# Kernel optimization log

Hardware: AMD Instinct MI355X
Metric: run time of the kernel (lower is better)

Reference implementation:

```python
import math
import jax, jax.numpy as jnp
import numpy as np

D_MODEL = 1024
D_FF = 4096
NUM_EXPERTS = 8
CAPACITY_FACTOR = 1.0
ALPHA = 0.01
Z_LOSS_COEF = 0.001


def setup_inputs() -> dict:
    key = jax.random.key(0)
    kx, kr, k1, k2, kb1, kb2 = jax.random.split(key, 6)
    init_scale = 0.1
    x = jax.random.normal(kx, (8, 2048, D_MODEL), dtype=jnp.float32)
    # torch Linear weight [out,in] with truncated-normal std=init_scale*sqrt(1/fan_in);
    # stored here in math layout: y = x @ W
    w_router = jax.random.normal(kr, (D_MODEL, NUM_EXPERTS), jnp.float32) * (init_scale * math.sqrt(1.0 / D_MODEL))
    w1 = jax.random.normal(k1, (NUM_EXPERTS, D_MODEL, D_FF), jnp.float32) * (init_scale * math.sqrt(1.0 / D_MODEL))
    w2 = jax.random.normal(k2, (NUM_EXPERTS, D_FF, D_MODEL), jnp.float32) * (init_scale * math.sqrt(1.0 / D_FF))
    b1 = jnp.zeros((NUM_EXPERTS, D_FF), jnp.float32)
    b2 = jnp.zeros((NUM_EXPERTS, D_MODEL), jnp.float32)
    return {"x": x, "w_router": w_router, "w1": w1, "b1": b1, "w2": w2, "b2": b2}


def reference(x, w_router, w1, b1, w2, b2):
    # Eval-mode forward (no router noise, no dropout), as in is_training=False.
    d = x.shape[-1]
    E = w1.shape[0]
    tokens = x.reshape(-1, d)                       # [T, d]
    T = tokens.shape[0]

    router_logits = tokens @ w_router               # [T, E]
    router_probs = jax.nn.softmax(router_logits.astype(jnp.float32), axis=-1)
    top1_prob = jnp.max(router_probs, axis=-1)      # [T]
    top1_idx = jnp.argmax(router_probs, axis=-1)    # [T]

    # load-balancing aux loss
    counts = jnp.zeros((E,), jnp.float32).at[top1_idx].add(1.0)
    fi = jax.lax.stop_gradient(counts / T)
    Pi = router_probs.mean(axis=0)
    aux_loss = ALPHA * E * jnp.dot(fi, Pi)
    z_loss = jnp.mean(jnp.square(jax.scipy.special.logsumexp(router_logits, axis=-1)))
    aux_loss = aux_loss + Z_LOSS_COEF * z_loss

    # capacity-limited first-come-first-serve positions per expert
    C = max(int(math.ceil(T / float(E) * CAPACITY_FACTOR)), 1)
    onehot = (top1_idx[:, None] == jnp.arange(E)[None, :]).astype(jnp.int32)  # [T, E]
    cum = jnp.cumsum(onehot, axis=0)
    pos = jnp.take_along_axis(cum, top1_idx[:, None], axis=1)[:, 0] - 1       # [T]
    fits = pos < C                                                            # [T]
    pos_c = jnp.clip(pos, 0, C - 1)

    # dispatch: dropped tokens contribute zeros (collision-safe add)
    contrib = tokens * fits[:, None].astype(tokens.dtype)
    expert_inputs = jnp.zeros((E, C, d), tokens.dtype).at[top1_idx, pos_c].add(contrib)

    # per-expert FFN as batched GEMMs
    h = jax.nn.relu(jnp.einsum('ecd,edf->ecf', expert_inputs, w1) + b1[:, None, :])
    expert_outputs = jnp.einsum('ecf,efd->ecd', h, w2) + b2[:, None, :]       # [E, C, d]

    # combine: fitted tokens get prob-weighted expert output, dropped tokens pass through
    gathered = expert_outputs[top1_idx, pos_c]                                # [T, d]
    scaled = gathered * top1_prob[:, None].astype(gathered.dtype)
    outputs_tokens = jnp.where(fits[:, None], scaled, tokens)
    return outputs_tokens.reshape(x.shape), aux_loss
```

## Files before the change

### kernel.cpp

```cpp
#include <hip/hip_runtime.h>
#include <stdint.h>
#include <stddef.h>

typedef __attribute__((ext_vector_type(4))) float floatx4;
typedef __attribute__((ext_vector_type(8))) int intx8;

#define T_TOK 16384
#define DM 1024
#define DF 4096
#define NE 8
#define CAP 2048

#define SCALE_ONE 127
#define SCALE_W   121

static __device__ __forceinline__ int pk4(float a, float b, float c, float d) {
  int v = __builtin_amdgcn_cvt_pk_fp8_f32(a, b, 0, false);
  v = __builtin_amdgcn_cvt_pk_fp8_f32(c, d, v, true);
  return v;
}

static __device__ __forceinline__ void async_cp16(const void* g, void* l) {
  typedef const unsigned int __attribute__((address_space(1)))* gp_t;
  typedef unsigned int __attribute__((address_space(3)))* lp_t;
  __builtin_amdgcn_global_load_lds((gp_t)g, (lp_t)l, 16, 0, 0);
}

__global__ void init_kernel(int* __restrict__ src_token) {
  int i = blockIdx.x * 256 + threadIdx.x;
  if (i < NE * CAP) src_token[i] = -1;
}

__global__ void __launch_bounds__(256, 4) router_kernel(
    const float* __restrict__ x, const float* __restrict__ wr,
    int* __restrict__ top_idx, float* __restrict__ top_prob,
    float* __restrict__ part) {
  __shared__ float wl[8][1024];
  __shared__ float bstat[4][12];
  int tid = threadIdx.x;
  int lane = tid & 63, w = tid >> 6;

#pragma unroll
  for (int r = 0; r < 8; r++) {
    int j = tid + 256 * r;
    float4 v = ((const float4*)wr)[j];
    int f = j >> 1;
    int e0 = (j & 1) * 4;
    wl[e0 + 0][f] = v.x;
    wl[e0 + 1][f] = v.y;
    wl[e0 + 2][f] = v.z;
    wl[e0 + 3][f] = v.w;
  }
  __syncthreads();

  int t0 = blockIdx.x * 8 + w * 2;

  float4 xa[2][4];
#pragma unroll
  for (int tok = 0; tok < 2; tok++)
#pragma unroll
    for (int i = 0; i < 4; i++)
      xa[tok][i] = *(const float4*)&x[(size_t)(t0 + tok) * DM + i * 256 + lane * 4];

  float acc[2][8];
#pragma unroll
  for (int tok = 0; tok < 2; tok++)
#pragma unroll
    for (int e = 0; e < 8; e++) acc[tok][e] = 0.f;

#pragma unroll
  for (int i = 0; i < 4; i++) {
    float4 wv[8];
#pragma unroll
    for (int e = 0; e < 8; e++)
      wv[e] = *(const float4*)&wl[e][i * 256 + lane * 4];
#pragma unroll
    for (int tok = 0; tok < 2; tok++) {
      float4 xv = xa[tok][i];
#pragma unroll
      for (int e = 0; e < 8; e++)
        acc[tok][e] = fmaf(xv.x, wv[e].x,
                      fmaf(xv.y, wv[e].y,
                      fmaf(xv.z, wv[e].z,
                      fmaf(xv.w, wv[e].w, acc[tok][e]))));
    }
  }

  float pi_acc[8] = {0, 0, 0, 0, 0, 0, 0, 0};
  float z_acc = 0.f;
#pragma unroll
  for (int tok = 0; tok < 2; tok++) {
    float a[8];
#pragma unroll
    for (int e = 0; e < 8; e++) a[e] = acc[tok][e];
#pragma unroll
    for (int off = 32; off > 0; off >>= 1)
#pragma unroll
      for (int e = 0; e < 8; e++) a[e] += __shfl_xor(a[e], off, 64);
    float mx = a[0]; int mi = 0;
#pragma unroll
    for (int e = 1; e < 8; e++) { if (a[e] > mx) { mx = a[e]; mi = e; } }
    float s = 0.f, pr[8];
#pragma unroll
    for (int e = 0; e < 8; e++) { pr[e] = __expf(a[e] - mx); s += pr[e]; }
    float inv = 1.f / s;
#pragma unroll
    for (int e = 0; e < 8; e++) pi_acc[e] += pr[e] * inv;
    float lse = mx + __logf(s);
    z_acc += lse * lse;
    if (lane == 0) { top_idx[t0 + tok] = mi; top_prob[t0 + tok] = pr[mi] * inv; }
  }

  if (lane == 0) {
#pragma unroll
    for (int e = 0; e < 8; e++) bstat[w][e] = pi_acc[e];
    bstat[w][8] = z_acc;
  }
  __syncthreads();
  if (tid < 9) {
    float s = bstat[0][tid] + bstat[1][tid] + bstat[2][tid] + bstat[3][tid];
    part[(size_t)blockIdx.x * 16 + tid] = s;
  }
}

__global__ void __launch_bounds__(1024) scan_kernel(
    const int* __restrict__ top_idx, const float* __restrict__ part,
    int* __restrict__ dest_slot, int* __restrict__ src_token,
    float* __restrict__ aux_out) {
  __shared__ int cnt[1024 * 9];
  __shared__ float sstat[16][12];
  int tid = threadIdx.x;

  float ps[9];
#pragma unroll
  for (int e = 0; e < 9; e++) ps[e] = 0.f;
#pragma unroll
  for (int rr = 0; rr < 2; rr++) {
    const float* pp = &part[(size_t)(tid + rr * 1024) * 16];
#pragma unroll
    for (int e = 0; e < 9; e++) ps[e] += pp[e];
  }
#pragma unroll
  for (int off = 32; off > 0; off >>= 1)
#pragma unroll
    for (int e = 0; e < 9; e++) ps[e] += __shfl_xor(ps[e], off, 64);
  if ((tid & 63) == 0) {
#pragma unroll
    for (int e = 0; e < 9; e++) sstat[tid >> 6][e] = ps[e];
  }

  int eloc[16];
  int c[8] = {0, 0, 0, 0, 0, 0, 0, 0};
#pragma unroll
  for (int i = 0; i < 16; i++) {
    int e = top_idx[tid * 16 + i];
    eloc[i] = e;
    c[e]++;
  }
#pragma unroll
  for (int e = 0; e < 8; e++) cnt[tid * 9 + e] = c[e];
  __syncthreads();
  for (int s = 1; s < 1024; s <<= 1) {
    int v[8];
    if (tid >= s) {
#pragma unroll
      for (int e = 0; e < 8; e++) v[e] = cnt[(tid - s) * 9 + e];
    }
    __syncthreads();
    if (tid >= s) {
#pragma unroll
      for (int e = 0; e < 8; e++) cnt[tid * 9 + e] += v[e];
    }
    __syncthreads();
  }
  int run[8];
#pragma unroll
  for (int e = 0; e < 8; e++) run[e] = cnt[tid * 9 + e] - c[e];
#pragma unroll
  for (int i = 0; i < 16; i++) {
    int t = tid * 16 + i;
    int e = eloc[i];
    int pos = run[e]++;
    int d = (pos < CAP) ? (e * CAP + pos) : -1;
    dest_slot[t] = d;
    if (d >= 0) src_token[d] = t;
  }
  if (tid == 1023) {
    float st[9];
#pragma unroll
    for (int e = 0; e < 9; e++) {
      float s = 0.f;
      for (int ww = 0; ww < 16; ww++) s += sstat[ww][e];
      st[e] = s;
    }
    float aux = 0.f;
    for (int e = 0; e < 8; e++)
      aux += ((float)cnt[1023 * 9 + e] / (float)T_TOK) * (st[e] / (float)T_TOK);
    aux = 0.01f * 8.f * aux + 0.001f * (st[8] / (float)T_TOK);
    *aux_out = aux;
  }
}

__global__ void __launch_bounds__(256) dispatch_kernel(
    const float* __restrict__ x, const int* __restrict__ src_token,
    unsigned char* __restrict__ A) {
  int slot = blockIdx.x;
  int tid = threadIdx.x;
  int src = src_token[slot];
  int v = 0;
  if (src >= 0) {
    float4 xv = *(const float4*)&x[(size_t)src * DM + tid * 4];
    v = pk4(xv.x, xv.y, xv.z, xv.w);
  }
  *(int*)&A[(size_t)slot * DM + tid * 4] = v;
}

__global__ void __launch_bounds__(256) transpose_cast_kernel(
    const float* __restrict__ src, unsigned char* __restrict__ dst,
    int K, int N) {
  __shared__ float tile[64][65];
  int e = blockIdx.z;
  int n0 = blockIdx.x * 64, k0 = blockIdx.y * 64;
  int tid = threadIdx.x;
  int tx = tid & 63, ty = tid >> 6;
  const float* S = src + (size_t)e * K * N;
  unsigned char* D = dst + (size_t)e * N * K;
#pragma unroll
  for (int r = 0; r < 16; r++) {
    int k = ty + r * 4;
    tile[k][tx] = S[(size_t)(k0 + k) * N + n0 + tx];
  }
  __syncthreads();
  int n = tid >> 2, kq = (tid & 3) * 16;
  int4 ov;
  int w[4];
#pragma unroll
  for (int g = 0; g < 4; g++) {
    int kk = kq + g * 4;
    w[g] = pk4(tile[kk + 0][n] * 64.f, tile[kk + 1][n] * 64.f,
               tile[kk + 2][n] * 64.f, tile[kk + 3][n] * 64.f);
  }
  ov.x = w[0]; ov.y = w[1]; ov.z = w[2]; ov.w = w[3];
  *(int4*)&D[(size_t)(n0 + n) * K + k0 + kq] = ov;
}


__global__ void __launch_bounds__(256) gemm1_kernel(
    const unsigned char* __restrict__ A, const unsigned char* __restrict__ BT,
    const float* __restrict__ b1, unsigned char* __restrict__ H) {
  __shared__ unsigned char As[128 * 128];
  __shared__ unsigned char Bs[128 * 128];
  int e = blockIdx.z;
  int n0 = blockIdx.x * 128, m0 = blockIdx.y * 128;
  const unsigned char* Ae = A + ((size_t)e * CAP + m0) * DM;
  const unsigned char* Be = BT + ((size_t)e * DF + n0) * DM;
  int tid = threadIdx.x;
  int lane = tid & 63, wid = tid >> 6;
  int wm = (wid & 1) * 64, wn = (wid >> 1) * 64;
  int l15 = lane & 15, q = lane >> 4;
  floatx4 acc[4][4];
#pragma unroll
  for (int i = 0; i < 4; i++)
#pragma unroll
    for (int j = 0; j < 4; j++) acc[i][j] = (floatx4){0.f, 0.f, 0.f, 0.f};
  for (int kb = 0; kb < DM; kb += 128) {
#pragma unroll
    for (int r = 0; r < 4; r++) {
      int c = tid + 256 * r;
      int row = c >> 3, cc = c & 7;
      int ccs = cc ^ (row & 7);
      async_cp16(Ae + (size_t)row * DM + kb + ccs * 16, As + c * 16);
      async_cp16(Be + (size_t)row * DM + kb + ccs * 16, Bs + c * 16);
    }
    __syncthreads();
    intx8 af[4], bf[4];
#pragma unroll
    for (int i = 0; i < 4; i++) {
      int row = wm + i * 16 + l15;
      int sw = row & 7;
      int4 lo = *(const int4*)&As[row * 128 + ((2 * q) ^ sw) * 16];
      int4 hi = *(const int4*)&As[row * 128 + ((2 * q + 1) ^ sw) * 16];
      af[i] = (intx8){lo.x, lo.y, lo.z, lo.w, hi.x, hi.y, hi.z, hi.w};
    }
#pragma unroll
    for (int j = 0; j < 4; j++) {
      int row = wn + j * 16 + l15;
      int sw = row & 7;
      int4 lo = *(const int4*)&Bs[row * 128 + ((2 * q) ^ sw) * 16];
      int4 hi = *(const int4*)&Bs[row * 128 + ((2 * q + 1) ^ sw) * 16];
      bf[j] = (intx8){lo.x, lo.y, lo.z, lo.w, hi.x, hi.y, hi.z, hi.w};
    }
#pragma unroll
    for (int i = 0; i < 4; i++)
#pragma unroll
      for (int j = 0; j < 4; j++)
        acc[i][j] = __builtin_amdgcn_mfma_scale_f32_16x16x128_f8f6f4(
            bf[j], af[i], acc[i][j], 0, 0, 0, SCALE_W, 0, SCALE_ONE);
    __syncthreads();
  }
  const float* b1e = b1 + e * DF;
#pragma unroll
  for (int i = 0; i < 4; i++) {
    int m = m0 + wm + i * 16 + l15;
    unsigned char* hrow = H + ((size_t)e * CAP + m) * DF;
#pragma unroll
    for (int j = 0; j < 4; j++) {
      int nb = n0 + wn + j * 16 + q * 4;
      float4 bv = *(const float4*)&b1e[nb];
      floatx4 a = acc[i][j];
      *(int*)&hrow[nb] = pk4(fmaxf(a[0] + bv.x, 0.f), fmaxf(a[1] + bv.y, 0.f),
                             fmaxf(a[2] + bv.z, 0.f), fmaxf(a[3] + bv.w, 0.f));
    }
  }
}

__global__ void __launch_bounds__(256) gemm2_kernel(
    const unsigned char* __restrict__ Hm, const unsigned char* __restrict__ BT,
    const float* __restrict__ b2, const int* __restrict__ src_token,
    const float* __restrict__ top_prob, float* __restrict__ out) {
  __shared__ unsigned char As[128 * 128];
  __shared__ unsigned char Bs[128 * 128];
  int e = blockIdx.z;
  int n0 = blockIdx.x * 128, m0 = blockIdx.y * 128;
  const unsigned char* Ae = Hm + ((size_t)e * CAP + m0) * DF;
  const unsigned char* Be = BT + ((size_t)e * DM + n0) * DF;
  int tid = threadIdx.x;
  int lane = tid & 63, wid = tid >> 6;
  int wm = (wid & 1) * 64, wn = (wid >> 1) * 64;
  int l15 = lane & 15, q = lane >> 4;
  floatx4 acc[4][4];
#pragma unroll
  for (int i = 0; i < 4; i++)
#pragma unroll
    for (int j = 0; j < 4; j++) acc[i][j] = (floatx4){0.f, 0.f, 0.f, 0.f};
  for (int kb = 0; kb < DF; kb += 128) {
#pragma unroll
    for (int r = 0; r < 4; r++) {
      int c = tid + 256 * r;
      int row = c >> 3, cc = c & 7;
      int ccs = cc ^ (row & 7);
      async_cp16(Ae + (size_t)row * DF + kb + ccs * 16, As + c * 16);
      async_cp16(Be + (size_t)row * DF + kb + ccs * 16, Bs + c * 16);
    }
    __syncthreads();
    intx8 af[4], bf[4];
#pragma unroll
    for (int i = 0; i < 4; i++) {
      int row = wm + i * 16 + l15;
      int sw = row & 7;
      int4 lo = *(const int4*)&As[row * 128 + ((2 * q) ^ sw) * 16];
      int4 hi = *(const int4*)&As[row * 128 + ((2 * q + 1) ^ sw) * 16];
      af[i] = (intx8){lo.x, lo.y, lo.z, lo.w, hi.x, hi.y, hi.z, hi.w};
    }
#pragma unroll
    for (int j = 0; j < 4; j++) {
      int row = wn + j * 16 + l15;
      int sw = row & 7;
      int4 lo = *(const int4*)&Bs[row * 128 + ((2 * q) ^ sw) * 16];
      int4 hi = *(const int4*)&Bs[row * 128 + ((2 * q + 1) ^ sw) * 16];
      bf[j] = (intx8){lo.x, lo.y, lo.z, lo.w, hi.x, hi.y, hi.z, hi.w};
    }
#pragma unroll
    for (int i = 0; i < 4; i++)
#pragma unroll
      for (int j = 0; j < 4; j++)
        acc[i][j] = __builtin_amdgcn_mfma_scale_f32_16x16x128_f8f6f4(
            bf[j], af[i], acc[i][j], 0, 0, 0, SCALE_W, 0, SCALE_ONE);
    __syncthreads();
  }
  const float* b2e = b2 + e * DM;
#pragma unroll
  for (int i = 0; i < 4; i++) {
    int m = m0 + wm + i * 16 + l15;
    int t = src_token[e * CAP + m];
    if (t < 0) continue;
    float p = top_prob[t];
    float* orow = out + (size_t)t * DM;
#pragma unroll
    for (int j = 0; j < 4; j++) {
      int nb = n0 + wn + j * 16 + q * 4;
      float4 bv = *(const float4*)&b2e[nb];
      floatx4 a = acc[i][j];
      float4 o;
      o.x = p * (a[0] + bv.x);
      o.y = p * (a[1] + bv.y);
      o.z = p * (a[2] + bv.z);
      o.w = p * (a[3] + bv.w);
      *(float4*)&orow[nb] = o;
    }
  }
}

__global__ void __launch_bounds__(256) passthru_kernel(
    const float* __restrict__ x, const int* __restrict__ dest_slot,
    float* __restrict__ out) {
  int t = blockIdx.x;
  if (dest_slot[t] >= 0) return;
  int c = threadIdx.x * 4;
  *(float4*)&out[(size_t)t * DM + c] = *(const float4*)&x[(size_t)t * DM + c];
}

extern "C" void kernel_launch(void* const* d_in, const int* in_sizes, int n_in,
                              void* d_out, int out_size, void* d_ws, size_t ws_size,
                              hipStream_t stream) {
  const float* x  = (const float*)d_in[0];
  const float* wr = (const float*)d_in[1];
  const float* w1 = (const float*)d_in[2];
  const float* b1 = (const float*)d_in[3];
  const float* w2 = (const float*)d_in[4];
  const float* b2 = (const float*)d_in[5];
  float* out = (float*)d_out;

  const size_t OFF_A    = 0;
  const size_t OFF_W1T  = 16777216;
  const size_t OFF_W2T  = 50331648;
  const size_t OFF_H    = 83886080;
  const size_t OFF_TIDX = 150994944;
  const size_t OFF_TPRB = 151060480;
  const size_t OFF_DEST = 151126016;
  const size_t OFF_SRC  = 151191552;
  const size_t OFF_STAT = 151257088;
  if (ws_size < OFF_STAT + 64) return;

  char* ws = (char*)d_ws;
  unsigned char* A_f8 = (unsigned char*)(ws + OFF_A);
  float* part = (float*)(ws + OFF_A);
  unsigned char* W1T  = (unsigned char*)(ws + OFF_W1T);
  unsigned char* W2T  = (unsigned char*)(ws + OFF_W2T);
  unsigned char* Hbuf = (unsigned char*)(ws + OFF_H);
  int*   top_idx   = (int*)(ws + OFF_TIDX);
  float* top_prob  = (float*)(ws + OFF_TPRB);
  int*   dest_slot = (int*)(ws + OFF_DEST);
  int*   src_token = (int*)(ws + OFF_SRC);

  hipLaunchKernelGGL(init_kernel, dim3(64), dim3(256), 0, stream, src_token);
  hipLaunchKernelGGL(router_kernel, dim3(2048), dim3(256), 0, stream,
                     x, wr, top_idx, top_prob, part);
  hipLaunchKernelGGL(scan_kernel, dim3(1), dim3(1024), 0, stream,
                     top_idx, part, dest_slot, src_token, out + (size_t)T_TOK * DM);
  hipLaunchKernelGGL(dispatch_kernel, dim3(NE * CAP), dim3(256), 0, stream,
                     x, src_token, A_f8);
  hipLaunchKernelGGL(transpose_cast_kernel, dim3(DF / 64, DM / 64, NE), dim3(256), 0, stream,
                     w1, W1T, DM, DF);
  hipLaunchKernelGGL(transpose_cast_kernel, dim3(DM / 64, DF / 64, NE), dim3(256), 0, stream,
                     w2, W2T, DF, DM);
  hipLaunchKernelGGL(gemm1_kernel, dim3(DF / 128, CAP / 128, NE), dim3(256), 0, stream,
                     A_f8, W1T, b1, Hbuf);
  hipLaunchKernelGGL(gemm2_kernel, dim3(DM / 128, CAP / 128, NE), dim3(256), 0, stream,
                     Hbuf, W2T, b2, src_token, top_prob, out);
  hipLaunchKernelGGL(passthru_kernel, dim3(T_TOK), dim3(256), 0, stream,
                     x, dest_slot, out);
}
```

Before: 638.6 us.

## Enlarge FP8 expert GEMM tiles to 256x256 with 8 waves and block swizzle

```diff
diff --git a/kernel.cpp b/kernel.cpp
--- a/kernel.cpp
+++ b/kernel.cpp
@@ -245,67 +245,74 @@
 }
 
 
-__global__ void __launch_bounds__(256) gemm1_kernel(
+__global__ void __launch_bounds__(512, 2) gemm1_kernel(
     const unsigned char* __restrict__ A, const unsigned char* __restrict__ BT,
     const float* __restrict__ b1, unsigned char* __restrict__ H) {
-  __shared__ unsigned char As[128 * 128];
-  __shared__ unsigned char Bs[128 * 128];
+  __shared__ __align__(16) unsigned char As[256 * 128];
+  __shared__ __align__(16) unsigned char Bs[256 * 128];
   int e = blockIdx.z;
-  int n0 = blockIdx.x * 128, m0 = blockIdx.y * 128;
+  int plane = blockIdx.x + 16 * blockIdx.y;
+  int nid = (plane & 7) * 16 + (plane >> 3);
+  int n0 = (nid & 15) * 256, m0 = (nid >> 4) * 256;
   const unsigned char* Ae = A + ((size_t)e * CAP + m0) * DM;
   const unsigned char* Be = BT + ((size_t)e * DF + n0) * DM;
   int tid = threadIdx.x;
   int lane = tid & 63, wid = tid >> 6;
-  int wm = (wid & 1) * 64, wn = (wid >> 1) * 64;
+  int wmi = wid >> 2, wni = wid & 3;
   int l15 = lane & 15, q = lane >> 4;
-  floatx4 acc[4][4];
-#pragma unroll
-  for (int i = 0; i < 4; i++)
+  floatx4 acc[8][4];
+#pragma unroll
+  for (int i = 0; i < 8; i++)
 #pragma unroll
     for (int j = 0; j < 4; j++) acc[i][j] = (floatx4){0.f, 0.f, 0.f, 0.f};
+
   for (int kb = 0; kb < DM; kb += 128) {
 #pragma unroll
     for (int r = 0; r < 4; r++) {
-      int c = tid + 256 * r;
+      int c = tid + 512 * r;
       int row = c >> 3, cc = c & 7;
       int ccs = cc ^ (row & 7);
       async_cp16(Ae + (size_t)row * DM + kb + ccs * 16, As + c * 16);
       async_cp16(Be + (size_t)row * DM + kb + ccs * 16, Bs + c * 16);
     }
     __syncthreads();
-    intx8 af[4], bf[4];
-#pragma unroll
-    for (int i = 0; i < 4; i++) {
-      int row = wm + i * 16 + l15;
-      int sw = row & 7;
-      int4 lo = *(const int4*)&As[row * 128 + ((2 * q) ^ sw) * 16];
-      int4 hi = *(const int4*)&As[row * 128 + ((2 * q + 1) ^ sw) * 16];
-      af[i] = (intx8){lo.x, lo.y, lo.z, lo.w, hi.x, hi.y, hi.z, hi.w};
-    }
+#pragma unroll
+    for (int ph = 0; ph < 4; ph++) {
+      const int Mh = ph >> 1, Nh = ph & 1;
+      intx8 af[4], bf[2];
+#pragma unroll
+      for (int i = 0; i < 4; i++) {
+        int row = wmi * 128 + (Mh * 4 + i) * 16 + l15;
+        int sw = row & 7;
+        int4 lo = *(const int4*)&As[row * 128 + ((2 * q) ^ sw) * 16];
+        int4 hi = *(const int4*)&As[row * 128 + ((2 * q + 1) ^ sw) * 16];
+        af[i] = (intx8){lo.x, lo.y, lo.z, lo.w, hi.x, hi.y, hi.z, hi.w};
+      }
+#pragma unroll
+      for (int j = 0; j < 2; j++) {
+        int row = wni * 64 + (Nh * 2 + j) * 16 + l15;
+        int sw = row & 7;
+        int4 lo = *(const int4*)&Bs[row * 128 + ((2 * q) ^ sw) * 16];
+        int4 hi = *(const int4*)&Bs[row * 128 + ((2 * q + 1) ^ sw) * 16];
+        bf[j] = (intx8){lo.x, lo.y, lo.z, lo.w, hi.x, hi.y, hi.z, hi.w};
+      }
+#pragma unroll
+      for (int i = 0; i < 4; i++)
+#pragma unroll
+        for (int j = 0; j < 2; j++)
+          acc[Mh * 4 + i][Nh * 2 + j] = __builtin_amdgcn_mfma_scale_f32_16x16x128_f8f6f4(
+              bf[j], af[i], acc[Mh * 4 + i][Nh * 2 + j], 0, 0, 0, SCALE_W, 0, SCALE_ONE);
+    }
+    __syncthreads();
+  }
+  const float* b1e = b1 + e * DF;
+#pragma unroll
+  for (int i = 0; i < 8; i++) {
+    int m = m0 + wmi * 128 + i * 16 + l15;
+    unsigned char* hrow = H + ((size_t)e * CAP + m) * DF;
 #pragma unroll
     for (int j = 0; j < 4; j++) {
-      int row = wn + j * 16 + l15;
-      int sw = row & 7;
-      int4 lo = *(const int4*)&Bs[row * 128 + ((2 * q) ^ sw) * 16];
-      int4 hi = *(const int4*)&Bs[row * 128 + ((2 * q + 1) ^ sw) * 16];
-      bf[j] = (intx8){lo.x, lo.y, lo.z, lo.w, hi.x, hi.y, hi.z, hi.w};
-    }
-#pragma unroll
-    for (int i = 0; i < 4; i++)
-#pragma unroll
-      for (int j = 0; j < 4; j++)
-        acc[i][j] = __builtin_amdgcn_mfma_scale_f32_16x16x128_f8f6f4(
-            bf[j], af[i], acc[i][j], 0, 0, 0, SCALE_W, 0, SCALE_ONE);
-    __syncthreads();
-  }
-  const float* b1e = b1 + e * DF;
-#pragma unroll
-  for (int i = 0; i < 4; i++) {
-    int m = m0 + wm + i * 16 + l15;
-    unsigned char* hrow = H + ((size_t)e * CAP + m) * DF;
-#pragma unroll
-    for (int j = 0; j < 4; j++) {
-      int nb = n0 + wn + j * 16 + q * 4;
+      int nb = n0 + wni * 64 + j * 16 + q * 4;
       float4 bv = *(const float4*)&b1e[nb];
       floatx4 a = acc[i][j];
       *(int*)&hrow[nb] = pk4(fmaxf(a[0] + bv.x, 0.f), fmaxf(a[1] + bv.y, 0.f),
@@ -314,71 +321,78 @@
   }
 }
 
-__global__ void __launch_bounds__(256) gemm2_kernel(
+__global__ void __launch_bounds__(512, 2) gemm2_kernel(
     const unsigned char* __restrict__ Hm, const unsigned char* __restrict__ BT,
     const float* __restrict__ b2, const int* __restrict__ src_token,
     const float* __restrict__ top_prob, float* __restrict__ out) {
-  __shared__ unsigned char As[128 * 128];
-  __shared__ unsigned char Bs[128 * 128];
+  __shared__ __align__(16) unsigned char As[256 * 128];
+  __shared__ __align__(16) unsigned char Bs[256 * 128];
   int e = blockIdx.z;
-  int n0 = blockIdx.x * 128, m0 = blockIdx.y * 128;
+  int plane = blockIdx.x + 4 * blockIdx.y;
+  int nid = (plane & 7) * 4 + (plane >> 3);
+  int n0 = (nid & 3) * 256, m0 = (nid >> 2) * 256;
   const unsigned char* Ae = Hm + ((size_t)e * CAP + m0) * DF;
   const unsigned char* Be = BT + ((size_t)e * DM + n0) * DF;
   int tid = threadIdx.x;
   int lane = tid & 63, wid = tid >> 6;
-  int wm = (wid & 1) * 64, wn = (wid >> 1) * 64;
+  int wmi = wid >> 2, wni = wid & 3;
   int l15 = lane & 15, q = lane >> 4;
-  floatx4 acc[4][4];
-#pragma unroll
-  for (int i = 0; i < 4; i++)
+  floatx4 acc[8][4];
+#pragma unroll
+  for (int i = 0; i < 8; i++)
 #pragma unroll
     for (int j = 0; j < 4; j++) acc[i][j] = (floatx4){0.f, 0.f, 0.f, 0.f};
+
   for (int kb = 0; kb < DF; kb += 128) {
 #pragma unroll
     for (int r = 0; r < 4; r++) {
-      int c = tid + 256 * r;
+      int c = tid + 512 * r;
       int row = c >> 3, cc = c & 7;
       int ccs = cc ^ (row & 7);
       async_cp16(Ae + (size_t)row * DF + kb + ccs * 16, As + c * 16);
       async_cp16(Be + (size_t)row * DF + kb + ccs * 16, Bs + c * 16);
     }
     __syncthreads();
-    intx8 af[4], bf[4];
-#pragma unroll
-    for (int i = 0; i < 4; i++) {
-      int row = wm + i * 16 + l15;
-      int sw = row & 7;
-      int4 lo = *(const int4*)&As[row * 128 + ((2 * q) ^ sw) * 16];
-      int4 hi = *(const int4*)&As[row * 128 + ((2 * q + 1) ^ sw) * 16];
-      af[i] = (intx8){lo.x, lo.y, lo.z, lo.w, hi.x, hi.y, hi.z, hi.w};
-    }
-#pragma unroll
-    for (int j = 0; j < 4; j++) {
-      int row = wn + j * 16 + l15;
-      int sw = row & 7;
-      int4 lo = *(const int4*)&Bs[row * 128 + ((2 * q) ^ sw) * 16];
-      int4 hi = *(const int4*)&Bs[row * 128 + ((2 * q + 1) ^ sw) * 16];
-      bf[j] = (intx8){lo.x, lo.y, lo.z, lo.w, hi.x, hi.y, hi.z, hi.w};
-    }
-#pragma unroll
-    for (int i = 0; i < 4; i++)
-#pragma unroll
-      for (int j = 0; j < 4; j++)
-        acc[i][j] = __builtin_amdgcn_mfma_scale_f32_16x16x128_f8f6f4(
-            bf[j], af[i], acc[i][j], 0, 0, 0, SCALE_W, 0, SCALE_ONE);
+#pragma unroll
+    for (int ph = 0; ph < 4; ph++) {
+      const int Mh = ph >> 1, Nh = ph & 1;
+      intx8 af[4], bf[2];
+#pragma unroll
+      for (int i = 0; i < 4; i++) {
+        int row = wmi * 128 + (Mh * 4 + i) * 16 + l15;
+        int sw = row & 7;
+        int4 lo = *(const int4*)&As[row * 128 + ((2 * q) ^ sw) * 16];
+        int4 hi = *(const int4*)&As[row * 128 + ((2 * q + 1) ^ sw) * 16];
+        af[i] = (intx8){lo.x, lo.y, lo.z, lo.w, hi.x, hi.y, hi.z, hi.w};
+      }
+#pragma unroll
+      for (int j = 0; j < 2; j++) {
+        int row = wni * 64 + (Nh * 2 + j) * 16 + l15;
+        int sw = row & 7;
+        int4 lo = *(const int4*)&Bs[row * 128 + ((2 * q) ^ sw) * 16];
+        int4 hi = *(const int4*)&Bs[row * 128 + ((2 * q + 1) ^ sw) * 16];
+        bf[j] = (intx8){lo.x, lo.y, lo.z, lo.w, hi.x, hi.y, hi.z, hi.w};
+      }
+#pragma unroll
+      for (int i = 0; i < 4; i++)
+#pragma unroll
+        for (int j = 0; j < 2; j++)
+          acc[Mh * 4 + i][Nh * 2 + j] = __builtin_amdgcn_mfma_scale_f32_16x16x128_f8f6f4(
+              bf[j], af[i], acc[Mh * 4 + i][Nh * 2 + j], 0, 0, 0, SCALE_W, 0, SCALE_ONE);
+    }
     __syncthreads();
   }
   const float* b2e = b2 + e * DM;
 #pragma unroll
-  for (int i = 0; i < 4; i++) {
-    int m = m0 + wm + i * 16 + l15;
+  for (int i = 0; i < 8; i++) {
+    int m = m0 + wmi * 128 + i * 16 + l15;
     int t = src_token[e * CAP + m];
     if (t < 0) continue;
     float p = top_prob[t];
     float* orow = out + (size_t)t * DM;
 #pragma unroll
     for (int j = 0; j < 4; j++) {
-      int nb = n0 + wn + j * 16 + q * 4;
+      int nb = n0 + wni * 64 + j * 16 + q * 4;
       float4 bv = *(const float4*)&b2e[nb];
       floatx4 a = acc[i][j];
       float4 o;
@@ -444,9 +458,9 @@
                      w1, W1T, DM, DF);
   hipLaunchKernelGGL(transpose_cast_kernel, dim3(DM / 64, DF / 64, NE), dim3(256), 0, stream,
                      w2, W2T, DF, DM);
-  hipLaunchKernelGGL(gemm1_kernel, dim3(DF / 128, CAP / 128, NE), dim3(256), 0, stream,
+  hipLaunchKernelGGL(gemm1_kernel, dim3(DF / 256, CAP / 256, NE), dim3(512), 0, stream,
                      A_f8, W1T, b1, Hbuf);
-  hipLaunchKernelGGL(gemm2_kernel, dim3(DM / 128, CAP / 128, NE), dim3(256), 0, stream,
+  hipLaunchKernelGGL(gemm2_kernel, dim3(DM / 256, CAP / 256, NE), dim3(512), 0, stream,
                      Hbuf, W2T, b2, src_token, top_prob, out);
   hipLaunchKernelGGL(passthru_kernel, dim3(T_TOK), dim3(256), 0, stream,
                      x, dest_slot, out);
```

After: 626.3 us. No clear change (-1.9%).
